# Optimization experiments

Measured on AMD Instinct MI355X. Metric: run time of the kernel, lower is better.

The kernel has to match this reference:

```python
import jax, jax.numpy as jnp
import numpy as np

EPS = 1e-5  # BatchNorm eps (torch default)


def setup_inputs() -> dict:
    key = jax.random.key(0)
    ks = jax.random.split(key, 12)
    B, T, F = 2048, 128, 84

    def rn(k, sh, scale=0.05):
        return jax.random.normal(k, sh, jnp.float32) * scale

    return {
        "x": jax.random.normal(ks[0], (B, T, F), jnp.float32),
        # Conv1d(84 -> 64, k=3, pad=1)
        "conv1d_w": rn(ks[1], (64, F, 3)),
        "conv1d_b": rn(ks[2], (64,)),
        # BatchNorm1d(64), eval mode (running stats)
        "bn_gamma": jnp.ones((64,), jnp.float32),
        "bn_beta": jnp.zeros((64,), jnp.float32),
        "bn_mean": jnp.zeros((64,), jnp.float32),
        "bn_var": jnp.ones((64,), jnp.float32),
        # Linear(64*16 -> 64*4*4)
        "lin_w": rn(ks[3], (1024, 1024)),
        "lin_b": rn(ks[4], (1024,)),
        # ConvLSTM cell: Conv2d(192 -> 512, k=3, pad=1, groups=4)
        "cell_w": rn(ks[5], (512, 48, 3, 3)),
        "cell_b": rn(ks[6], (512,)),
        # Classifier
        "cls1_w": rn(ks[7], (128, 2048)),
        "cls1_b": rn(ks[8], (128,)),
        "cls2_w": rn(ks[9], (2, 128)),
        "cls2_b": rn(ks[10], (2,)),
    }


def reference(x, conv1d_w, conv1d_b, bn_gamma, bn_beta, bn_mean, bn_var,
              lin_w, lin_b, cell_w, cell_b, cls1_w, cls1_b, cls2_w, cls2_b):
    B, T, F = x.shape
    H = 128  # hidden channels

    # Per-timestep encoder is state-free -> vectorize over (B, T).
    # Conv1d k=3 pad=1 on a length-1 sequence: only the center tap hits data.
    enc = jnp.einsum('btf,cf->btc', x, conv1d_w[:, :, 1]) + conv1d_b  # [B,T,64]
    enc = (enc - bn_mean) * (bn_gamma / jnp.sqrt(bn_var + EPS)) + bn_beta
    enc = jax.nn.relu(enc)
    # flatten of [64,16] is channel-major -> repeat along last axis.
    flat = jnp.repeat(enc, 16, axis=-1)                               # [B,T,1024]
    to2d = jnp.einsum('btk,ok->bto', flat, lin_w) + lin_b             # [B,T,1024]
    xt = to2d.reshape(B, T, 64, 4, 4).transpose(1, 0, 2, 3, 4)        # [T,B,64,4,4]

    def step(carry, x_t):
        h, c = carry
        comb = jnp.concatenate([x_t, h], axis=1)                      # [B,192,4,4]
        conv = jax.lax.conv_general_dilated(
            comb, cell_w, window_strides=(1, 1), padding='SAME',
            dimension_numbers=('NCHW', 'OIHW', 'NCHW'),
            feature_group_count=4)
        conv = conv + cell_b[None, :, None, None]                     # [B,512,4,4]
        cc_i, cc_f, cc_o, cc_g = jnp.split(conv, 4, axis=1)
        c_next = jax.nn.sigmoid(cc_f) * c + jax.nn.sigmoid(cc_i) * jnp.tanh(cc_g)
        h_next = jax.nn.sigmoid(cc_o) * jnp.tanh(c_next)
        return (h_next, c_next), None

    h0 = jnp.zeros((B, H, 4, 4), x.dtype)
    (h_last, _), _ = jax.lax.scan(step, (h0, h0), xt)

    feat = h_last.reshape(B, H * 16)                                  # [B,2048]
    hid = jax.nn.relu(feat @ cls1_w.T + cls1_b)
    return hid @ cls2_w.T + cls2_b                                    # [B,2]
```

## Files before the change

### kernel.cpp

```cpp
#include <hip/hip_runtime.h>
#include <math.h>

#define BN_EPS 1e-5f

typedef _Float16 f16x8 __attribute__((ext_vector_type(8)));
typedef _Float16 f16x4 __attribute__((ext_vector_type(4)));
typedef _Float16 f16x2 __attribute__((ext_vector_type(2)));
typedef unsigned short u16x8 __attribute__((ext_vector_type(8)));
typedef float f32x4 __attribute__((ext_vector_type(4)));
typedef float f32x16 __attribute__((ext_vector_type(16)));


__global__ void prep_enc_w(const float* __restrict__ conv1d_w,
                           const float* __restrict__ conv1d_b,
                           const float* __restrict__ gamma,
                           const float* __restrict__ beta,
                           const float* __restrict__ mean,
                           const float* __restrict__ var,
                           float* __restrict__ We, float* __restrict__ be) {
  int tid = blockIdx.x * blockDim.x + threadIdx.x;
  if (tid < 5376) {
    int c = tid / 84, f = tid % 84;
    float s = gamma[c] * rsqrtf(var[c] + BN_EPS);
    We[c * 84 + f] = s * conv1d_w[c * 252 + f * 3 + 1];
    if (f == 0) be[c] = s * conv1d_b[c] + (beta[c] - mean[c] * s);
  }
}

__global__ void prep_wef(const float* __restrict__ We, _Float16* __restrict__ WeF) {
  int tid = blockIdx.x * blockDim.x + threadIdx.x;
  if (tid >= 6144) return;
  int j = tid & 7, lane = (tid >> 3) & 63, kch = (tid >> 9) % 3, ct = tid / 1536;
  int c = ct * 16 + (lane & 15);
  int k = kch * 32 + (lane >> 4) * 8 + j;
  WeF[tid] = (k < 84) ? (_Float16)We[c * 84 + k] : (_Float16)0.f;
}

__global__ void prep_w2(const float* __restrict__ lin_w, float* __restrict__ W2) {
  int tid = blockIdx.x * blockDim.x + threadIdx.x;
  int o2 = tid >> 6, c = tid & 63;
  float s = 0.f;
#pragma unroll
  for (int j = 0; j < 16; ++j) s += lin_w[o2 * 1024 + c * 16 + j];
  W2[o2 * 64 + c] = s;
}

__global__ void prep_A(const float* __restrict__ cell_w,
                       const float* __restrict__ cell_b,
                       const float* __restrict__ lin_b,
                       const float* __restrict__ W2,
                       float* __restrict__ A, float* __restrict__ Abias) {
  int tid = blockIdx.x * blockDim.x + threadIdx.x;
  int go = tid >> 10;
  int c = (tid >> 4) & 63;
  int p = tid & 15;
  int y = p >> 2, x = p & 3;
  int kn = (go >= 128) ? 16 : 48;
  int xb = (go >= 128) ? 48 : 0;
  float a = 0.f;
  for (int k = 0; k < kn; ++k)
    for (int dy = 0; dy < 3; ++dy) {
      int yy = y + dy - 1;
      if (yy < 0 || yy > 3) continue;
      for (int dx = 0; dx < 3; ++dx) {
        int xx = x + dx - 1;
        if (xx < 0 || xx > 3) continue;
        a += cell_w[((go * 48 + k) * 3 + dy) * 3 + dx] *
             W2[((xb + k) * 16 + yy * 4 + xx) * 64 + c];
      }
    }
  A[(go * 64 + c) * 16 + p] = a;
  if (c == 0) {
    float bs = cell_b[go];
    for (int k = 0; k < kn; ++k)
      for (int dy = 0; dy < 3; ++dy) {
        int yy = y + dy - 1;
        if (yy < 0 || yy > 3) continue;
        for (int dx = 0; dx < 3; ++dx) {
          int xx = x + dx - 1;
          if (xx < 0 || xx > 3) continue;
          bs += cell_w[((go * 48 + k) * 3 + dy) * 3 + dx] *
                lin_b[(xb + k) * 16 + yy * 4 + xx];
        }
      }
    Abias[go * 16 + p] = bs;
  }
}

__global__ void pack_a16(const float* __restrict__ A, _Float16* __restrict__ Apk) {
  int tid = blockIdx.x * blockDim.x + threadIdx.x;
  int j = tid & 7, lane = (tid >> 3) & 63, kch = (tid >> 9) & 1, go = tid >> 10;
  int p = lane & 15;
  int c = kch * 32 + (lane >> 4) * 8 + j;
  Apk[tid] = (_Float16)A[(go * 64 + c) * 16 + p];
}

__global__ void pack_wcv(const float* __restrict__ cell_w, _Float16* __restrict__ Wcv) {
  int tid = blockIdx.x * blockDim.x + threadIdx.x;
  int j = tid & 7, lane = (tid >> 3) & 63, m = (tid >> 9) & 3, tmk = tid >> 11;
  int co = m * 32 + (lane & 31);
  int khi = (lane >> 5) * 8 + j;
  float v;
  if (tmk < 18) {
    int kch = tmk / 9, tap = tmk % 9;
    v = cell_w[((size_t)(128 + co) * 48 + 16 + kch * 16 + khi) * 9 + tap];
  } else if (tmk < 45) {
    int r = tmk - 18; int kch = r / 9, tap = r % 9;
    v = cell_w[((size_t)(256 + co) * 48 + kch * 16 + khi) * 9 + tap];
  } else {
    int r = tmk - 45; int kch = r / 9, tap = r % 9;
    v = cell_w[((size_t)(384 + co) * 48 + kch * 16 + khi) * 9 + tap];
  }
  Wcv[tid] = (_Float16)v;
}

__device__ __forceinline__ float sigm(float v) {
  return __fdividef(1.f, 1.f + __expf(-v));
}
__device__ __forceinline__ float tanh_fast(float v) {
  return 1.f - __fdividef(2.f, __expf(2.f * v) + 1.f);
}

__global__ __launch_bounds__(256, 3) void xgate_kernel(
    const float* __restrict__ x, const _Float16* __restrict__ WeF,
    const float* __restrict__ be, const _Float16* __restrict__ Apk,
    const float* __restrict__ Abias, unsigned short* __restrict__ sixf, int tc) {
  __shared__ __align__(16) _Float16 x16[128 * 104];
  __shared__ __align__(16) _Float16 enc_s[128 * 72];
  __shared__ __align__(16) unsigned char Tt[4 * 2304];
  int tid = threadIdx.x, lane = tid & 63, w = tid >> 6;
  int gq = blockIdx.x >> 7, cq = blockIdx.x & 127;
  int n = lane & 15, kgrp = lane >> 4;

  {
    int r = tid >> 1, half = tid & 1;
    int b = cq * 16 + (r >> 3), t = tc * 8 + (r & 7);
    const float* rowp = x + ((size_t)b * 128 + t) * 84;
#pragma unroll
    for (int j = 0; j < 11; ++j) {
      int q = half + 2 * j;
      if (q < 21) {
        float4 v = *(const float4*)(rowp + q * 4);
        f16x4 h;
        h[0] = (_Float16)v.x; h[1] = (_Float16)v.y;
        h[2] = (_Float16)v.z; h[3] = (_Float16)v.w;
        *(f16x4*)(&x16[r * 104 + q * 4]) = h;
      }
    }
    for (int i = tid; i < 4096; i += 256) {
      int rr = i >> 5, k = i & 31;
      if (k < 20) x16[rr * 104 + 84 + k] = (_Float16)0.f;
    }
  }
  __syncthreads();

  for (int ct4 = 0; ct4 < 8; ++ct4) {
    f32x4 acc = *(const f32x4*)(be + w * 16 + kgrp * 4);
#pragma unroll
    for (int kch = 0; kch < 3; ++kch)
      acc = __builtin_amdgcn_mfma_f32_16x16x32_f16(
          *(const f16x8*)(WeF + ((w * 3 + kch) * 64 + lane) * 8),
          *(const f16x8*)(&x16[(ct4 * 16 + n) * 104 + kch * 32 + kgrp * 8]),
          acc, 0, 0, 0);
#pragma unroll
    for (int r = 0; r < 4; ++r)
      enc_s[(ct4 * 16 + n) * 72 + w * 16 + kgrp * 4 + r] =
          (_Float16)fmaxf(acc[r], 0.f);
  }
  __syncthreads();

  int slotB = gq >> 1;
  int chbase = (gq & 1) * 64 + w * 16;
  unsigned char* Tw = Tt + w * 2304;
  int fn = lane >> 2;
  for (int ct4 = 0; ct4 < 8; ++ct4) {
    int ccl = ct4 * 16 + n;
    int fb = cq * 16 + ct4 * 2 + (fn >> 3), ftr = fn & 7;
    size_t grow =
        (((size_t)fb * 8 + ftr) * 2 + slotB) * 2048 + (size_t)chbase * 16;
    for (int gb = 0; gb < 4; ++gb) {
#pragma unroll
      for (int gi = 0; gi < 4; ++gi) {
        int gol = gb * 4 + gi;
        int go = gq * 64 + w * 16 + gol;
        f32x4 acc = *(const f32x4*)(Abias + go * 16 + kgrp * 4);
        acc = __builtin_amdgcn_mfma_f32_16x16x32_f16(
            *(const f16x8*)(Apk + (size_t)go * 1024 + lane * 8),
            *(const f16x8*)(&enc_s[ccl * 72 + kgrp * 8]), acc, 0, 0, 0);
        acc = __builtin_amdgcn_mfma_f32_16x16x32_f16(
            *(const f16x8*)(Apk + (size_t)go * 1024 + 512 + lane * 8),
            *(const f16x8*)(&enc_s[ccl * 72 + 32 + kgrp * 8]), acc, 0, 0, 0);
        unsigned char* tdst = Tw + n * 144 + gi * 32 + kgrp * 8;
        if (gq < 2) {
#pragma unroll
          for (int rp = 0; rp < 2; ++rp) {
            unsigned lo = (unsigned)(sigm(acc[rp * 2]) * 65535.f + 0.5f);
            unsigned hi = (unsigned)(sigm(acc[rp * 2 + 1]) * 65535.f + 0.5f);
            *(unsigned*)(tdst + rp * 4) = lo | (hi << 16);
          }
        } else {
#pragma unroll
          for (int rp = 0; rp < 2; ++rp) {
            f16x2 pv = {(_Float16)acc[rp * 2], (_Float16)acc[rp * 2 + 1]};
            *(f16x2*)(tdst + rp * 4) = pv;
          }
        }
      }
      asm volatile("s_waitcnt lgkmcnt(0)" ::: "memory");
      __builtin_amdgcn_sched_barrier(0);
#pragma unroll
      for (int j = 0; j < 2; ++j) {
        int chunk = (lane & 3) + 4 * j;
        f16x8 v = *(const f16x8*)(Tw + fn * 144 + chunk * 16);
        *(f16x8*)(sixf + grow + (size_t)gb * 64 + (size_t)chunk * 8) = v;
      }
      asm volatile("s_waitcnt lgkmcnt(0)" ::: "memory");
      __builtin_amdgcn_sched_barrier(0);
    }
  }
}

#define HPB 4624
#define HPQ 272
#define ZQ 4352
#define COFF 36992
#define GOFF 102528
#define GSZ 18432
#define LDSZ 157824

__device__ __forceinline__ void cell_update(
    unsigned char* lds, const unsigned short* __restrict__ sixf_b,
    _Float16* __restrict__ h16_b, int ch, int bl, int hf, int t,
    float cbo, float cbg, bool lastT) {
  int b = hf * 4 + bl;
  int cell = hf * 512 + ch * 4 + bl;
  const unsigned short* sp = sixf_b + ((size_t)b * 8 + t) * 4096 + ch * 16;
  u16x8 s0 = *(const u16x8*)(sp);
  u16x8 s1 = *(const u16x8*)(sp + 8);
  f16x8 x0 = *(const f16x8*)(sp + 2048);
  f16x8 x1 = *(const f16x8*)(sp + 2056);
  const _Float16* Gf = (const _Float16*)(lds + GOFF + 0 * GSZ + ch * 144 + bl * 32);
  const _Float16* Go = (const _Float16*)(lds + GOFF + 1 * GSZ + ch * 144 + bl * 32);
  const _Float16* Gg = (const _Float16*)(lds + GOFF + 2 * GSZ + ch * 144 + bl * 32);
  float* cp = (float*)(lds + COFF) + cell;
#pragma unroll
  for (int h8 = 0; h8 < 2; ++h8) {
    u16x8 s = h8 ? s1 : s0;
    f16x8 xv = h8 ? x1 : x0;
    f16x8 gfv = *(const f16x8*)(Gf + h8 * 8);
    f16x8 gov = *(const f16x8*)(Go + h8 * 8);
    f16x8 ggv = *(const f16x8*)(Gg + h8 * 8);
#pragma unroll
    for (int j = 0; j < 8; ++j) {
      int p = h8 * 8 + j;
      float si = (float)s[j] * (1.f / 65535.f);
      float xf = (float)xv[j];
      float cold = cp[p * 1024];
      float cv = sigm(xf + (float)gfv[j]) * cold +
                 si * tanh_fast(cbg + (float)ggv[j]);
      cp[p * 1024] = cv;
      float hn = sigm(cbo + (float)gov[j]) * tanh_fast(cv);
      *(_Float16*)(lds + b * HPB + p * HPQ + ch * 2) = (_Float16)hn;
      if (lastT) h16_b[((size_t)b * 16 + p) * 128 + ch] = (_Float16)hn;
    }
  }
}

template <int GATE>
__device__ __forceinline__ void role_loop(
    unsigned char* lds, const _Float16* __restrict__ Wg,
    const unsigned short* __restrict__ sixf_b,
    _Float16* __restrict__ h16_b, const float* __restrict__ cell_b,
    int m, int lane, int tid, const unsigned* tapbase, unsigned gwbase) {
  constexpr int NKCH = (GATE == 0) ? 2 : 3;
  constexpr unsigned CIOFF = (GATE == 0) ? 0u : (GATE == 1 ? 64u : 160u);
  f16x8 wr[NKCH * 9];
#pragma unroll
  for (int fi = 0; fi < NKCH * 9; ++fi)
    wr[fi] = *(const f16x8*)(Wg + (size_t)(fi * 4 + m) * 512 + (lane << 3));

  int idx = (GATE == 2) ? (tid - 256) : tid;
  int ch = idx >> 2, bl = idx & 3;
  constexpr bool own0 = (GATE != 2), own1 = (GATE != 1);
  float cbo = cell_b[256 + ch], cbg = cell_b[384 + ch];

  for (int t = 0; t < 8; ++t) {
#pragma unroll
    for (int hf = 0; hf < 2; ++hf) {
#pragma unroll
      for (int nt = 0; nt < 2; ++nt) {
        unsigned bofs = (unsigned)(hf * 4 + nt * 2) * HPB;
        f32x16 acc = {};
#pragma unroll
        for (int kch = 0; kch < NKCH; ++kch)
#pragma unroll
          for (int tap = 0; tap < 9; ++tap)
            acc = __builtin_amdgcn_mfma_f32_32x32x16_f16(
                wr[kch * 9 + tap],
                *(const f16x8*)(lds + tapbase[tap] + bofs + CIOFF +
                                (unsigned)kch * 32),
                acc, 0, 0, 0);
#pragma unroll
        for (int r = 0; r < 16; ++r) {
          unsigned co_l = (unsigned)((r & 3) + 8 * (r >> 2));
          *(_Float16*)(lds + gwbase + (unsigned)GATE * GSZ + co_l * 144u +
                       (unsigned)nt * 64u) = (_Float16)acc[r];
        }
      }
      __syncthreads();
      if (hf == 0) {
        if (own0) cell_update(lds, sixf_b, h16_b, ch, bl, 0, t, cbo, cbg, t == 7);
      } else {
        if (own1) cell_update(lds, sixf_b, h16_b, ch, bl, 1, t, cbo, cbg, t == 7);
      }
      __syncthreads();
    }
  }
}

__global__ __launch_bounds__(768, 3) void recur8_kernel(
    const unsigned short* __restrict__ sixf, const _Float16* __restrict__ Wcv,
    const float* __restrict__ cell_b, _Float16* __restrict__ h16,
    float* __restrict__ cstate) {
  __shared__ __align__(16) unsigned char lds[LDSZ];
  int tid = threadIdx.x, lane = tid & 63, w = tid >> 6;
  int gate = w >> 2, m = w & 3;

  _Float16* h16_b = h16 + (size_t)blockIdx.x * 16384;
  for (int i = tid; i < 16384; i += 768) {
    int bl8 = i >> 11, q = (i >> 7) & 15, chh = i & 127;
    *(_Float16*)(lds + bl8 * HPB + q * HPQ + chh * 2) = h16_b[i];
  }
  for (int i = tid; i < 1024; i += 768) {
    int bl8 = i >> 7, chh = i & 127;
    *(_Float16*)(lds + bl8 * HPB + ZQ + chh * 2) = (_Float16)0.f;
  }
  float* cl = (float*)(lds + COFF);
  float* cst_b = cstate + (size_t)blockIdx.x * 16384;
  for (int i = tid; i < 16384; i += 768) cl[i] = cst_b[i];

  int col = lane & 31, khalf = lane >> 5, b_lo = col >> 4, p_c = col & 15;
  int yc = p_c >> 2, xc = p_c & 3;
  unsigned tapbase[9];
#pragma unroll
  for (int dy = 0; dy < 3; ++dy)
#pragma unroll
    for (int dx = 0; dx < 3; ++dx) {
      int qy = yc + dy - 1, qx = xc + dx - 1;
      bool valid = (qy >= 0 && qy < 4 && qx >= 0 && qx < 4);
      tapbase[dy * 3 + dx] =
          (valid ? (unsigned)((qy * 4 + qx) * HPQ) : (unsigned)ZQ) +
          (unsigned)(b_lo * HPB + khalf * 16);
    }
  unsigned gwbase = (unsigned)GOFF + (unsigned)((m * 32 + khalf * 4) * 144) +
                    (unsigned)(b_lo * 32 + p_c * 2);
  __syncthreads();

  const unsigned short* sixf_b = sixf + (size_t)blockIdx.x * 262144;
  if (gate == 0)
    role_loop<0>(lds, Wcv, sixf_b, h16_b, cell_b, m, lane, tid, tapbase, gwbase);
  else if (gate == 1)
    role_loop<1>(lds, Wcv + 36864, sixf_b, h16_b, cell_b, m, lane, tid, tapbase, gwbase);
  else
    role_loop<2>(lds, Wcv + 92160, sixf_b, h16_b, cell_b, m, lane, tid, tapbase, gwbase);

  for (int i = tid; i < 16384; i += 768) cst_b[i] = cl[i];
}

__global__ __launch_bounds__(128) void cls_kernel(
    const _Float16* __restrict__ h16, const float* __restrict__ w1,
    const float* __restrict__ b1, const float* __restrict__ w2,
    const float* __restrict__ b2, float* __restrict__ out) {
  __shared__ __align__(16) float feat[8 * 2064];
  __shared__ float hid[8 * 128];
  int b0 = blockIdx.x * 8;
  for (int i = threadIdx.x; i < 16384; i += 128) {
    int bl = i >> 11, r = i & 2047, p = r >> 7, chh = r & 127;
    feat[bl * 2064 + chh * 16 + p] = (float)h16[(size_t)b0 * 2048 + i];
  }
  __syncthreads();
  int ch = threadIdx.x;
  float acc[8];
#pragma unroll
  for (int b = 0; b < 8; ++b) acc[b] = b1[ch];
  const float4* wr = (const float4*)(w1 + (size_t)ch * 2048);
  for (int k4 = 0; k4 < 512; ++k4) {
    float4 wv = wr[k4];
#pragma unroll
    for (int b = 0; b < 8; ++b) {
      float4 f = *(const float4*)(&feat[b * 2064 + k4 * 4]);
      acc[b] += wv.x * f.x + wv.y * f.y + wv.z * f.z + wv.w * f.w;
    }
  }
#pragma unroll
  for (int b = 0; b < 8; ++b) hid[b * 128 + ch] = fmaxf(acc[b], 0.f);
  __syncthreads();
  if (threadIdx.x < 16) {
    int b = threadIdx.x >> 1, o = threadIdx.x & 1;
    float s = b2[o];
    for (int k = 0; k < 128; ++k) s += hid[b * 128 + k] * w2[o * 128 + k];
    out[(size_t)(b0 + b) * 2 + o] = s;
  }
}

extern "C" void kernel_launch(void* const* d_in, const int* in_sizes, int n_in,
                              void* d_out, int out_size, void* d_ws, size_t ws_size,
                              hipStream_t stream) {
  const float* x        = (const float*)d_in[0];
  const float* conv1d_w = (const float*)d_in[1];
  const float* conv1d_b = (const float*)d_in[2];
  const float* bn_gamma = (const float*)d_in[3];
  const float* bn_beta  = (const float*)d_in[4];
  const float* bn_mean  = (const float*)d_in[5];
  const float* bn_var   = (const float*)d_in[6];
  const float* lin_w    = (const float*)d_in[7];
  const float* lin_b    = (const float*)d_in[8];
  const float* cell_w   = (const float*)d_in[9];
  const float* cell_b   = (const float*)d_in[10];
  const float* cls1_w   = (const float*)d_in[11];
  const float* cls1_b   = (const float*)d_in[12];
  const float* cls2_w   = (const float*)d_in[13];
  const float* cls2_b   = (const float*)d_in[14];

  float* ws = (float*)d_ws;
  float* We    = ws + 0;
  float* be    = ws + 8192;
  float* W2    = ws + 12288;
  float* A     = ws + 81920;
  float* Abias = ws + 344064;
  _Float16* WeF = (_Float16*)(ws + 348160);
  _Float16* Apk = (_Float16*)(ws + 352256);
  _Float16* Wcv = (_Float16*)(ws + 483328);
  _Float16* h16 = (_Float16*)(ws + 557056);
  float* cstate = ws + 2654208;
  unsigned short* sixf = (unsigned short*)(ws + 6848512);
  float* out = (float*)d_out;

  prep_enc_w<<<21, 256, 0, stream>>>(conv1d_w, conv1d_b, bn_gamma, bn_beta,
                                     bn_mean, bn_var, We, be);
  prep_wef<<<24, 256, 0, stream>>>(We, WeF);
  prep_w2<<<256, 256, 0, stream>>>(lin_w, W2);
  prep_A<<<1024, 256, 0, stream>>>(cell_w, cell_b, lin_b, W2, A, Abias);
  pack_a16<<<1024, 256, 0, stream>>>(A, Apk);
  pack_wcv<<<576, 256, 0, stream>>>(cell_w, Wcv);
  hipMemsetAsync(h16, 0, 8388608, stream);
  hipMemsetAsync(cstate, 0, 16777216, stream);
  for (int tc = 0; tc < 16; ++tc) {
    xgate_kernel<<<512, 256, 0, stream>>>(x, WeF, be, Apk, Abias, sixf, tc);
    recur8_kernel<<<256, 768, 0, stream>>>(sixf, Wcv, cell_b, h16, cstate);
  }
  cls_kernel<<<256, 128, 0, stream>>>(h16, cls1_w, cls1_b, cls2_w, cls2_b, out);
}
```

Before: 3.513 ms.

## Pipeline ConvLSTM cell update with next gate MFMA tile across all waves

The recurrent loop now runs over 32 (timestep, half, n-tile) stages instead of separate conv and update phases. Each stage runs the elementwise gate update for the previous two-batch tile while the MFMAs for the current tile are issued. The update is spread over all 768 threads, one cell element per item. Previously only two thirds of the waves did the update and they sat idle during the conv. The cell state moves to a new per-tile LDS layout, and the gate biases now come from LDS. The cost is scalar, non-vectorised LDS and global loads in the update.

```diff
diff --git a/kernel.cpp b/kernel.cpp
--- a/kernel.cpp
+++ b/kernel.cpp
@@ -226,40 +226,36 @@
 #define COFF 36992
 #define GOFF 102528
 #define GSZ 18432
-#define LDSZ 157824
-
-__device__ __forceinline__ void cell_update(
+#define CBOFF 157824
+#define LDSZ 158848
+
+__device__ __forceinline__ void update_items(
     unsigned char* lds, const unsigned short* __restrict__ sixf_b,
-    _Float16* __restrict__ h16_b, int ch, int bl, int hf, int t,
-    float cbo, float cbg, bool lastT) {
-  int b = hf * 4 + bl;
-  int cell = hf * 512 + ch * 4 + bl;
-  const unsigned short* sp = sixf_b + ((size_t)b * 8 + t) * 4096 + ch * 16;
-  u16x8 s0 = *(const u16x8*)(sp);
-  u16x8 s1 = *(const u16x8*)(sp + 8);
-  f16x8 x0 = *(const f16x8*)(sp + 2048);
-  f16x8 x1 = *(const f16x8*)(sp + 2056);
-  const _Float16* Gf = (const _Float16*)(lds + GOFF + 0 * GSZ + ch * 144 + bl * 32);
-  const _Float16* Go = (const _Float16*)(lds + GOFF + 1 * GSZ + ch * 144 + bl * 32);
-  const _Float16* Gg = (const _Float16*)(lds + GOFF + 2 * GSZ + ch * 144 + bl * 32);
-  float* cp = (float*)(lds + COFF) + cell;
-#pragma unroll
-  for (int h8 = 0; h8 < 2; ++h8) {
-    u16x8 s = h8 ? s1 : s0;
-    f16x8 xv = h8 ? x1 : x0;
-    f16x8 gfv = *(const f16x8*)(Gf + h8 * 8);
-    f16x8 gov = *(const f16x8*)(Go + h8 * 8);
-    f16x8 ggv = *(const f16x8*)(Gg + h8 * 8);
-#pragma unroll
-    for (int j = 0; j < 8; ++j) {
-      int p = h8 * 8 + j;
-      float si = (float)s[j] * (1.f / 65535.f);
-      float xf = (float)xv[j];
-      float cold = cp[p * 1024];
-      float cv = sigm(xf + (float)gfv[j]) * cold +
-                 si * tanh_fast(cbg + (float)ggv[j]);
-      cp[p * 1024] = cv;
-      float hn = sigm(cbo + (float)gov[j]) * tanh_fast(cv);
+    _Float16* __restrict__ h16_b, int tid, int q) {
+  int tP = q >> 2, hfP = (q >> 1) & 1, ntP = q & 1;
+  bool lastT = (tP == 7);
+  float* cbase = (float*)(lds + COFF) + (hfP * 2 + ntP) * 4096;
+#pragma unroll 2
+  for (int k = 0; k < 6; ++k) {
+    int item = tid + k * 768;
+    if (item < 4096) {
+      int cell = item >> 4, p = item & 15;
+      int ch = cell & 127, blbit = cell >> 7;
+      int b = hfP * 4 + ntP * 2 + blbit;
+      const unsigned short* sp =
+          sixf_b + ((size_t)b * 8 + tP) * 4096 + ch * 16 + p;
+      float si = (float)sp[0] * (1.f / 65535.f);
+      float xf = (float)*(const _Float16*)(sp + 2048);
+      unsigned gbyte = (unsigned)(ch * 144 + ntP * 64 + blbit * 32 + p * 2);
+      float gf = (float)*(const _Float16*)(lds + GOFF + 0 * GSZ + gbyte);
+      float go = (float)*(const _Float16*)(lds + GOFF + 1 * GSZ + gbyte);
+      float gg = (float)*(const _Float16*)(lds + GOFF + 2 * GSZ + gbyte);
+      float cbo = *(const float*)(lds + CBOFF + ch * 4);
+      float cbg = *(const float*)(lds + CBOFF + 512 + ch * 4);
+      float* cp = cbase + cell * 16 + p;
+      float cv = sigm(xf + gf) * cp[0] + si * tanh_fast(cbg + gg);
+      cp[0] = cv;
+      float hn = sigm(cbo + go) * tanh_fast(cv);
       *(_Float16*)(lds + b * HPB + p * HPQ + ch * 2) = (_Float16)hn;
       if (lastT) h16_b[((size_t)b * 16 + p) * 128 + ch] = (_Float16)hn;
     }
@@ -270,7 +266,7 @@
 __device__ __forceinline__ void role_loop(
     unsigned char* lds, const _Float16* __restrict__ Wg,
     const unsigned short* __restrict__ sixf_b,
-    _Float16* __restrict__ h16_b, const float* __restrict__ cell_b,
+    _Float16* __restrict__ h16_b,
     int m, int lane, int tid, const unsigned* tapbase, unsigned gwbase) {
   constexpr int NKCH = (GATE == 0) ? 2 : 3;
   constexpr unsigned CIOFF = (GATE == 0) ? 0u : (GATE == 1 ? 64u : 160u);
@@ -279,43 +275,30 @@
   for (int fi = 0; fi < NKCH * 9; ++fi)
     wr[fi] = *(const f16x8*)(Wg + (size_t)(fi * 4 + m) * 512 + (lane << 3));
 
-  int idx = (GATE == 2) ? (tid - 256) : tid;
-  int ch = idx >> 2, bl = idx & 3;
-  constexpr bool own0 = (GATE != 2), own1 = (GATE != 1);
-  float cbo = cell_b[256 + ch], cbg = cell_b[384 + ch];
-
-  for (int t = 0; t < 8; ++t) {
-#pragma unroll
-    for (int hf = 0; hf < 2; ++hf) {
-#pragma unroll
-      for (int nt = 0; nt < 2; ++nt) {
-        unsigned bofs = (unsigned)(hf * 4 + nt * 2) * HPB;
-        f32x16 acc = {};
-#pragma unroll
-        for (int kch = 0; kch < NKCH; ++kch)
-#pragma unroll
-          for (int tap = 0; tap < 9; ++tap)
-            acc = __builtin_amdgcn_mfma_f32_32x32x16_f16(
-                wr[kch * 9 + tap],
-                *(const f16x8*)(lds + tapbase[tap] + bofs + CIOFF +
-                                (unsigned)kch * 32),
-                acc, 0, 0, 0);
-#pragma unroll
-        for (int r = 0; r < 16; ++r) {
-          unsigned co_l = (unsigned)((r & 3) + 8 * (r >> 2));
-          *(_Float16*)(lds + gwbase + (unsigned)GATE * GSZ + co_l * 144u +
-                       (unsigned)nt * 64u) = (_Float16)acc[r];
-        }
-      }
-      __syncthreads();
-      if (hf == 0) {
-        if (own0) cell_update(lds, sixf_b, h16_b, ch, bl, 0, t, cbo, cbg, t == 7);
-      } else {
-        if (own1) cell_update(lds, sixf_b, h16_b, ch, bl, 1, t, cbo, cbg, t == 7);
-      }
-      __syncthreads();
-    }
-  }
+  for (int q = 0; q < 32; ++q) {
+    if (q > 0) update_items(lds, sixf_b, h16_b, tid, q - 1);
+    int hf = (q >> 1) & 1, nt = q & 1;
+    unsigned bofs = (unsigned)(hf * 4 + nt * 2) * HPB;
+    f32x16 acc = {};
+#pragma unroll
+    for (int kch = 0; kch < NKCH; ++kch)
+#pragma unroll
+      for (int tap = 0; tap < 9; ++tap)
+        acc = __builtin_amdgcn_mfma_f32_32x32x16_f16(
+            wr[kch * 9 + tap],
+            *(const f16x8*)(lds + tapbase[tap] + bofs + CIOFF +
+                            (unsigned)kch * 32),
+            acc, 0, 0, 0);
+#pragma unroll
+    for (int r = 0; r < 16; ++r) {
+      unsigned co_l = (unsigned)((r & 3) + 8 * (r >> 2));
+      *(_Float16*)(lds + gwbase + (unsigned)GATE * GSZ + co_l * 144u +
+                   (unsigned)nt * 64u) = (_Float16)acc[r];
+    }
+    __syncthreads();
+  }
+  update_items(lds, sixf_b, h16_b, tid, 31);
+  __syncthreads();
 }
 
 __global__ __launch_bounds__(768, 3) void recur8_kernel(
@@ -338,6 +321,7 @@
   float* cl = (float*)(lds + COFF);
   float* cst_b = cstate + (size_t)blockIdx.x * 16384;
   for (int i = tid; i < 16384; i += 768) cl[i] = cst_b[i];
+  if (tid < 256) *(float*)(lds + CBOFF + tid * 4) = cell_b[256 + tid];
 
   int col = lane & 31, khalf = lane >> 5, b_lo = col >> 4, p_c = col & 15;
   int yc = p_c >> 2, xc = p_c & 3;
@@ -358,11 +342,11 @@
 
   const unsigned short* sixf_b = sixf + (size_t)blockIdx.x * 262144;
   if (gate == 0)
-    role_loop<0>(lds, Wcv, sixf_b, h16_b, cell_b, m, lane, tid, tapbase, gwbase);
+    role_loop<0>(lds, Wcv, sixf_b, h16_b, m, lane, tid, tapbase, gwbase);
   else if (gate == 1)
-    role_loop<1>(lds, Wcv + 36864, sixf_b, h16_b, cell_b, m, lane, tid, tapbase, gwbase);
+    role_loop<1>(lds, Wcv + 36864, sixf_b, h16_b, m, lane, tid, tapbase, gwbase);
   else
-    role_loop<2>(lds, Wcv + 92160, sixf_b, h16_b, cell_b, m, lane, tid, tapbase, gwbase);
+    role_loop<2>(lds, Wcv + 92160, sixf_b, h16_b, m, lane, tid, tapbase, gwbase);
 
   for (int i = tid; i < 16384; i += 768) cst_b[i] = cl[i];
 }
```

New measurement: 3.651 ms. +3.9%, slower.
